# Optimization experiments

Hardware: AMD Instinct MI355X
Metric: run time of the kernel (lower is better)

Reference implementation:

```python
import jax, jax.numpy as jnp
import numpy as np

B, N, C = 4, 2048, 768
H = 12
HD = C // H  # 64
SCALE = HD ** -0.5


def setup_inputs() -> dict:
    key = jax.random.key(0)
    ks = jax.random.split(key, 3)
    x = jax.random.normal(ks[0], (B, N, C), dtype=jnp.float32)
    w_qkv = jax.random.normal(ks[1], (C, 3 * C), dtype=jnp.float32) * (C ** -0.5)
    b_qkv = jnp.zeros((3 * C,), dtype=jnp.float32)
    w_proj = jax.random.normal(ks[2], (C, C), dtype=jnp.float32) * (C ** -0.5)
    b_proj = jnp.zeros((C,), dtype=jnp.float32)
    return {"x": x, "w_qkv": w_qkv, "b_qkv": b_qkv, "w_proj": w_proj, "b_proj": b_proj}


def reference(x, w_qkv, b_qkv, w_proj, b_proj):
    # fused QKV projection: [B, N, 3C] -> [3, B, H, N, HD]
    qkv = (x @ w_qkv + b_qkv).reshape(B, N, 3, H, HD).transpose(2, 0, 3, 1, 4)
    q, k, v = qkv[0] * SCALE, qkv[1], qkv[2]
    # scores [B, H, N, N] (Global mixer: no mask)
    attn = jnp.einsum('bhnd,bhmd->bhnm', q, k)
    attn = jax.nn.softmax(attn, axis=-1)
    # attn @ V -> [B, N, C]
    out = jnp.einsum('bhnm,bhmd->bhnd', attn, v).transpose(0, 2, 1, 3).reshape(B, N, C)
    return out @ w_proj + b_proj
```

## Files before the change

kernel.cpp:

```cpp
#include <hip/hip_runtime.h>
#include <hip/hip_bf16.h>
#include <math.h>

#define B_ 4
#define N_ 2048
#define C_ 768
#define H_ 12
#define HD_ 64

typedef short short8 __attribute__((ext_vector_type(8)));
typedef float float16v __attribute__((ext_vector_type(16)));
typedef unsigned short u16;
typedef unsigned int u32;

static __device__ __forceinline__ u16 f2bf(float x) {
    __hip_bfloat16 b = __float2bfloat16(x);
    return *reinterpret_cast<u16*>(&b);
}
#if defined(__has_builtin)
#if __has_builtin(__builtin_amdgcn_exp2f)
#define EXP2F_FAST __builtin_amdgcn_exp2f
#endif
#endif
#ifndef EXP2F_FAST
#define EXP2F_FAST exp2f
#endif
static __device__ __forceinline__ u32 cpk(float lo, float hi) {
    u32 r;
    asm("v_cvt_pk_bf16_f32 %0, %1, %2" : "=v"(r) : "v"(lo), "v"(hi));
    return r;
}
static __device__ __forceinline__ void gload_lds16(const u16* g, u16* l) {
    __builtin_amdgcn_global_load_lds(
        (const __attribute__((address_space(1))) void*)g,
        (__attribute__((address_space(3))) void*)l, 16, 0, 0);
}

__global__ __launch_bounds__(256) void cast_bf16_kernel(
    const float* __restrict__ X, u16* __restrict__ Xb, int n4)
{
    int i = blockIdx.x * 256 + threadIdx.x;
    if (i < n4) {
        float4 v = ((const float4*)X)[i];
        uint2 o = make_uint2(cpk(v.x, v.y), cpk(v.z, v.w));
        ((uint2*)Xb)[i] = o;
    }
}

__global__ __launch_bounds__(256) void transpose_cvt_kernel(
    const float* __restrict__ W, u16* __restrict__ Wt, int R, int Cc)
{
    __shared__ float tile[64][65];
    const int t = threadIdx.x;
    const int r0 = blockIdx.y * 64, c0 = blockIdx.x * 64;
    const int tr = t >> 4, tc = (t & 15) * 4;
#pragma unroll
    for (int i = 0; i < 4; i++) {
        float4 v = *(const float4*)(W + (size_t)(r0 + tr + i * 16) * Cc + c0 + tc);
        tile[tr + i * 16][tc + 0] = v.x;
        tile[tr + i * 16][tc + 1] = v.y;
        tile[tr + i * 16][tc + 2] = v.z;
        tile[tr + i * 16][tc + 3] = v.w;
    }
    __syncthreads();
#pragma unroll
    for (int i = 0; i < 4; i++) {
        int n = tr + i * 16;
        int k = tc;
        uint2 o = make_uint2(cpk(tile[k + 0][n], tile[k + 1][n]),
                             cpk(tile[k + 2][n], tile[k + 3][n]));
        *(uint2*)(Wt + (size_t)(c0 + n) * R + r0 + k) = o;
    }
}

template<bool OUT_BF16, bool BIAS_ROW>
__global__ __launch_bounds__(256) void gemm_mfma_kernel(
    const u16* __restrict__ A, int lda,
    const u16* __restrict__ Bt,
    const float* __restrict__ bias,
    void* __restrict__ C, int ldc,
    int K, float scale, int scale_cols)
{
    __shared__ u16 As[128 * 64];
    __shared__ u16 Bs[128 * 64];
    const int t = threadIdx.x;
    const int w = t >> 6, lane = t & 63, ln = lane & 31, e = lane >> 5;
    const int wm = w >> 1, wn = w & 1;
    const int row0 = blockIdx.y * 128, col0 = blockIdx.x * 128;
    const int r_sub = lane >> 3;
    const int cg = (lane & 7) ^ r_sub;

    float16v acc[2][2];
#pragma unroll
    for (int i = 0; i < 16; i++) {
        acc[0][0][i] = 0.f; acc[0][1][i] = 0.f;
        acc[1][0][i] = 0.f; acc[1][1][i] = 0.f;
    }

    for (int k0 = 0; k0 < K; k0 += 64) {
        __syncthreads();
#pragma unroll
        for (int i = 0; i < 4; i++) {
            int rr = w * 32 + i * 8;
            const u16* ga = A + (size_t)(row0 + rr + r_sub) * lda + k0 + cg * 8;
            gload_lds16(ga, As + rr * 64);
            const u16* gb = Bt + (size_t)(col0 + rr + r_sub) * K + k0 + cg * 8;
            gload_lds16(gb, Bs + rr * 64);
        }
        __syncthreads();

#pragma unroll
        for (int ks = 0; ks < 4; ks++) {
            short8 af[2], bf[2];
#pragma unroll
            for (int sm = 0; sm < 2; sm++) {
                int r = wm * 64 + sm * 32 + ln;
                af[sm] = *(const short8*)&As[r * 64 + ((2 * ks + e) ^ (r & 7)) * 8];
            }
#pragma unroll
            for (int sn = 0; sn < 2; sn++) {
                int r = wn * 64 + sn * 32 + ln;
                bf[sn] = *(const short8*)&Bs[r * 64 + ((2 * ks + e) ^ (r & 7)) * 8];
            }
#pragma unroll
            for (int sm = 0; sm < 2; sm++)
#pragma unroll
                for (int sn = 0; sn < 2; sn++)
                    acc[sm][sn] = __builtin_amdgcn_mfma_f32_32x32x16_bf16(
                        af[sm], bf[sn], acc[sm][sn], 0, 0, 0);
        }
    }

    const float sc = (col0 < scale_cols) ? scale : 1.0f;
#pragma unroll
    for (int sm = 0; sm < 2; sm++)
#pragma unroll
        for (int sn = 0; sn < 2; sn++) {
            int col = col0 + wn * 64 + sn * 32 + ln;
            float bvc = BIAS_ROW ? 0.f : bias[col];
#pragma unroll
            for (int reg = 0; reg < 16; reg++) {
                int row = row0 + wm * 64 + sm * 32 + (reg & 3) + 8 * (reg >> 2) + 4 * e;
                float bv = BIAS_ROW ? bias[row] : bvc;
                float v = (acc[sm][sn][reg] + bv) * sc;
                if (OUT_BF16)
                    ((u16*)C)[(size_t)row * ldc + col] = f2bf(v);
                else
                    ((float*)C)[(size_t)row * ldc + col] = v;
            }
        }
}

__global__ __launch_bounds__(256) void attn_kernel(
    const u16* __restrict__ qk, const u16* __restrict__ Vt, u16* __restrict__ Ob)
{
    __shared__ __align__(16) u16 lds_us[17664];

    const int t = threadIdx.x;
    const int w = t >> 6, lane = t & 63, ln = lane & 31, e = lane >> 5;
    const int rt = w & 1, kt = w >> 1;
    const int r_sub = lane >> 3;
    const int cgk = (lane & 7) ^ r_sub;

    const int bid = blockIdx.x;
    const int xcd = bid & 7, j = bid >> 3;
    const int bh = xcd * 6 + (j >> 4);
    const int b = bh / H_, h = bh % H_;
    const int row0 = (j & 15) * 128;

    const u16* kq0 = qk + (size_t)b * N_ * 1536 + 768 + h * 64 + cgk * 8
                        + (size_t)(w * 16 + r_sub) * 1536;
    const u16* kq1 = kq0 + (size_t)8 * 1536;
    const u16* vq0 = Vt + (size_t)(h * 64 + w * 16 + r_sub) * (B_ * N_)
                        + b * N_ + cgk * 8;
    const u16* vq1 = vq0 + (size_t)8 * (B_ * N_);

    {
        u16* Kp = lds_us;
        u16* Vp = lds_us + 4096;
        gload_lds16(kq0, Kp + (w * 16 + 0) * 64);
        gload_lds16(kq1, Kp + (w * 16 + 8) * 64);
        gload_lds16(vq0, Vp + (w * 16 + 0) * 64);
        gload_lds16(vq1, Vp + (w * 16 + 8) * 64);
        kq0 += (size_t)64 * 1536; kq1 += (size_t)64 * 1536;
        vq0 += 64; vq1 += 64;
    }

    short8 qfA[4], qfB[4];
    {
        const u16* qa = qk + (size_t)(b * N_ + row0 + rt * 64 + ln) * 1536 + h * 64;
#pragma unroll
        for (int ks = 0; ks < 4; ks++) {
            qfA[ks] = __builtin_bit_cast(short8, *(const uint4*)(qa + ks * 16 + e * 8));
            qfB[ks] = __builtin_bit_cast(short8, *(const uint4*)(qa + 32 * 1536 + ks * 16 + e * 8));
        }
    }

    float16v accA0, accA1, accB0, accB1;
#pragma unroll
    for (int i = 0; i < 16; i++) { accA0[i] = 0.f; accA1[i] = 0.f; accB0[i] = 0.f; accB1[i] = 0.f; }
    float lA = 0.f, lB = 0.f;

    for (int c = 0; c < N_ / 64; c++) {
        __syncthreads();
        if (c + 1 < N_ / 64) {
            u16* Kp = lds_us + ((c + 1) & 1) * 8192;
            u16* Vp = Kp + 4096;
            gload_lds16(kq0, Kp + (w * 16 + 0) * 64);
            gload_lds16(kq1, Kp + (w * 16 + 8) * 64);
            gload_lds16(vq0, Vp + (w * 16 + 0) * 64);
            gload_lds16(vq1, Vp + (w * 16 + 8) * 64);
            kq0 += (size_t)64 * 1536; kq1 += (size_t)64 * 1536;
            vq0 += 64; vq1 += 64;
        }
        const u16* Ks = lds_us + (c & 1) * 8192;
        const u16* Vs = Ks + 4096;

        float16v sA, sB;
#pragma unroll
        for (int i = 0; i < 16; i++) { sA[i] = 0.f; sB[i] = 0.f; }
        const int krow = kt * 32 + ln;
#pragma unroll
        for (int ks = 0; ks < 4; ks++) {
            int slot = (2 * ks + e) ^ (ln & 7);
            short8 kf = *(const short8*)&Ks[krow * 64 + slot * 8];
            sA = __builtin_amdgcn_mfma_f32_32x32x16_bf16(kf, qfA[ks], sA, 0, 0, 0);
            sB = __builtin_amdgcn_mfma_f32_32x32x16_bf16(kf, qfB[ks], sB, 0, 0, 0);
        }

#pragma unroll
        for (int i = 0; i < 16; i++) {
            sA[i] = EXP2F_FAST(sA[i]);
            sB[i] = EXP2F_FAST(sB[i]);
        }
        {
            float a0 = (sA[0] + sA[1]) + (sA[2] + sA[3]);
            float a1 = (sA[4] + sA[5]) + (sA[6] + sA[7]);
            float a2 = (sA[8] + sA[9]) + (sA[10] + sA[11]);
            float a3 = (sA[12] + sA[13]) + (sA[14] + sA[15]);
            float b0 = (sB[0] + sB[1]) + (sB[2] + sB[3]);
            float b1 = (sB[4] + sB[5]) + (sB[6] + sB[7]);
            float b2 = (sB[8] + sB[9]) + (sB[10] + sB[11]);
            float b3 = (sB[12] + sB[13]) + (sB[14] + sB[15]);
            float la = (a0 + a1) + (a2 + a3);
            float lb = (b0 + b1) + (b2 + b3);
            lA += la + __shfl_xor(la, 32);
            lB += lb + __shfl_xor(lb, 32);
        }

#pragma unroll
        for (int g2 = 0; g2 < 2; g2++) {
            uint4 pA4 = make_uint4(cpk(sA[8 * g2 + 0], sA[8 * g2 + 1]),
                                   cpk(sA[8 * g2 + 2], sA[8 * g2 + 3]),
                                   cpk(sA[8 * g2 + 4], sA[8 * g2 + 5]),
                                   cpk(sA[8 * g2 + 6], sA[8 * g2 + 7]));
            uint4 pB4 = make_uint4(cpk(sB[8 * g2 + 0], sB[8 * g2 + 1]),
                                   cpk(sB[8 * g2 + 2], sB[8 * g2 + 3]),
                                   cpk(sB[8 * g2 + 4], sB[8 * g2 + 5]),
                                   cpk(sB[8 * g2 + 6], sB[8 * g2 + 7]));
            short8 pfA = __builtin_bit_cast(short8, pA4);
            short8 pfB = __builtin_bit_cast(short8, pB4);

            const int c0 = 4 * kt + 2 * g2;
#pragma unroll
            for (int dh = 0; dh < 2; dh++) {
                int d = dh * 32 + ln;
                uint2 r1 = *(const uint2*)&Vs[d * 64 + ((c0 ^ (d & 7)) * 8) + 4 * e];
                uint2 r2 = *(const uint2*)&Vs[d * 64 + (((c0 + 1) ^ (d & 7)) * 8) + 4 * e];
                uint4 va4 = make_uint4(r1.x, r1.y, r2.x, r2.y);
                short8 va = __builtin_bit_cast(short8, va4);
                if (dh == 0) {
                    accA0 = __builtin_amdgcn_mfma_f32_32x32x16_bf16(va, pfA, accA0, 0, 0, 0);
                    accB0 = __builtin_amdgcn_mfma_f32_32x32x16_bf16(va, pfB, accB0, 0, 0, 0);
                } else {
                    accA1 = __builtin_amdgcn_mfma_f32_32x32x16_bf16(va, pfA, accA1, 0, 0, 0);
                    accB1 = __builtin_amdgcn_mfma_f32_32x32x16_bf16(va, pfB, accB1, 0, 0, 0);
                }
            }
        }
    }

    __syncthreads();
    float* Osf = (float*)lds_us;
    float* lred = Osf + 128 * 68;
    const int rowA = rt * 64 + ln, rowB = rt * 64 + 32 + ln;

    if (kt == 1) {
#pragma unroll
        for (int reg = 0; reg < 16; reg++) {
            int d = (reg & 3) + 8 * (reg >> 2) + 4 * e;
            Osf[rowA * 68 + d]      = accA0[reg];
            Osf[rowA * 68 + d + 32] = accA1[reg];
            Osf[rowB * 68 + d]      = accB0[reg];
            Osf[rowB * 68 + d + 32] = accB1[reg];
        }
        lred[rowA] = lA;
        lred[rowB] = lB;
    }
    __syncthreads();
    if (kt == 0) {
        float linvA = 1.0f / (lA + lred[rowA]);
        float linvB = 1.0f / (lB + lred[rowB]);
#pragma unroll
        for (int reg = 0; reg < 16; reg++) {
            int d = (reg & 3) + 8 * (reg >> 2) + 4 * e;
            Osf[rowA * 68 + d]      = (accA0[reg] + Osf[rowA * 68 + d]) * linvA;
            Osf[rowA * 68 + d + 32] = (accA1[reg] + Osf[rowA * 68 + d + 32]) * linvA;
            Osf[rowB * 68 + d]      = (accB0[reg] + Osf[rowB * 68 + d]) * linvB;
            Osf[rowB * 68 + d + 32] = (accB1[reg] + Osf[rowB * 68 + d + 32]) * linvB;
        }
#pragma unroll
        for (int j2 = 0; j2 < 8; j2++) {
            int idx = lane + j2 * 64;
            int r = idx >> 3, gg = idx & 7;
            float4 o0 = *(float4*)&Osf[(rt * 64 + r) * 68 + gg * 8];
            float4 o1 = *(float4*)&Osf[(rt * 64 + r) * 68 + gg * 8 + 4];
            uint4 ov = make_uint4(cpk(o0.x, o0.y), cpk(o0.z, o0.w),
                                  cpk(o1.x, o1.y), cpk(o1.z, o1.w));
            *(uint4*)(Ob + (size_t)(b * N_ + row0 + rt * 64 + r) * 768
                         + h * 64 + gg * 8) = ov;
        }
    }
}

extern "C" void kernel_launch(void* const* d_in, const int* in_sizes, int n_in,
                              void* d_out, int out_size, void* d_ws, size_t ws_size,
                              hipStream_t stream) {
    const float* x      = (const float*)d_in[0];
    const float* w_qkv  = (const float*)d_in[1];
    const float* b_qkv  = (const float*)d_in[2];
    const float* w_proj = (const float*)d_in[3];
    const float* b_proj = (const float*)d_in[4];
    float* out = (float*)d_out;

    char* ws = (char*)d_ws;
    u16* qk2    = (u16*)ws;
    u16* Vt     = (u16*)(ws + 25165824);
    u16* Ob     = (u16*)(ws + 37748736);
    u16* xb     = (u16*)(ws + 50331648);
    u16* wqkvT  = (u16*)(ws + 62914560);
    u16* wprojT = (u16*)(ws + 66453504);

    cast_bf16_kernel<<<6144, 256, 0, stream>>>(x, xb, (B_ * N_ * C_) / 4);
    transpose_cvt_kernel<<<dim3(36, 12), 256, 0, stream>>>(w_qkv, wqkvT, C_, 3 * C_);
    transpose_cvt_kernel<<<dim3(12, 12), 256, 0, stream>>>(w_proj, wprojT, C_, C_);

    gemm_mfma_kernel<true, false><<<dim3(12, 64), 256, 0, stream>>>(
        xb, C_, wqkvT, b_qkv, qk2, 1536, C_, 0.18033688011112042f, 768);

    gemm_mfma_kernel<true, true><<<dim3(64, 6), 256, 0, stream>>>(
        wqkvT + (size_t)1536 * C_, C_, xb, b_qkv + 1536, Vt, B_ * N_, C_, 1.0f, 0);

    attn_kernel<<<768, 256, 0, stream>>>(qk2, Vt, Ob);

    gemm_mfma_kernel<false, false><<<dim3(6, 64), 256, 0, stream>>>(
        Ob, C_, wprojT, b_proj, out, C_, C_, 1.0f, 0);
}
```

Baseline: 234.5 us.

## Load K/V directly from global into registers instead of LDS staging

The attention kernel stops staging K and V tiles in double-buffered shared memory with per-iteration barriers. Each wave now loads its own K rows and V slices straight into registers, prefetching K one iteration ahead, and shared memory is kept only for the final cross-wave reduction. Launch bounds now request three blocks per CU. This removes barriers and LDS traffic but duplicates global loads across waves and uses narrow strided V reads, raising register pressure and memory traffic.

```diff
diff --git a/kernel.cpp b/kernel.cpp
--- a/kernel.cpp
+++ b/kernel.cpp
@@ -151,16 +151,15 @@
         }
 }
 
-__global__ __launch_bounds__(256) void attn_kernel(
+__global__ __launch_bounds__(256, 3) void attn_kernel(
     const u16* __restrict__ qk, const u16* __restrict__ Vt, u16* __restrict__ Ob)
 {
-    __shared__ __align__(16) u16 lds_us[17664];
+    __shared__ float Osf[128 * 68];
+    __shared__ float lred[128];
 
     const int t = threadIdx.x;
     const int w = t >> 6, lane = t & 63, ln = lane & 31, e = lane >> 5;
     const int rt = w & 1, kt = w >> 1;
-    const int r_sub = lane >> 3;
-    const int cgk = (lane & 7) ^ r_sub;
 
     const int bid = blockIdx.x;
     const int xcd = bid & 7, j = bid >> 3;
@@ -168,23 +167,9 @@
     const int b = bh / H_, h = bh % H_;
     const int row0 = (j & 15) * 128;
 
-    const u16* kq0 = qk + (size_t)b * N_ * 1536 + 768 + h * 64 + cgk * 8
-                        + (size_t)(w * 16 + r_sub) * 1536;
-    const u16* kq1 = kq0 + (size_t)8 * 1536;
-    const u16* vq0 = Vt + (size_t)(h * 64 + w * 16 + r_sub) * (B_ * N_)
-                        + b * N_ + cgk * 8;
-    const u16* vq1 = vq0 + (size_t)8 * (B_ * N_);
-
-    {
-        u16* Kp = lds_us;
-        u16* Vp = lds_us + 4096;
-        gload_lds16(kq0, Kp + (w * 16 + 0) * 64);
-        gload_lds16(kq1, Kp + (w * 16 + 8) * 64);
-        gload_lds16(vq0, Vp + (w * 16 + 0) * 64);
-        gload_lds16(vq1, Vp + (w * 16 + 8) * 64);
-        kq0 += (size_t)64 * 1536; kq1 += (size_t)64 * 1536;
-        vq0 += 64; vq1 += 64;
-    }
+    const u16* kp = qk + (size_t)(b * N_ + 32 * kt + ln) * 1536 + 768 + h * 64 + e * 8;
+    const u16* vpl = Vt + (size_t)(h * 64 + ln) * (B_ * N_) + b * N_ + 32 * kt + 4 * e;
+    const u16* vph = vpl + (size_t)32 * (B_ * N_);
 
     short8 qfA[4], qfB[4];
     {
@@ -201,31 +186,50 @@
     for (int i = 0; i < 16; i++) { accA0[i] = 0.f; accA1[i] = 0.f; accB0[i] = 0.f; accB1[i] = 0.f; }
     float lA = 0.f, lB = 0.f;
 
+    uint4 k0 = *(const uint4*)(kp + 0 * 16);
+    uint4 k1 = *(const uint4*)(kp + 1 * 16);
+    uint4 k2 = *(const uint4*)(kp + 2 * 16);
+    uint4 k3 = *(const uint4*)(kp + 3 * 16);
+    kp += (size_t)64 * 1536;
+
     for (int c = 0; c < N_ / 64; c++) {
-        __syncthreads();
+        uint2 vv[2][2][2];
+#pragma unroll
+        for (int dh = 0; dh < 2; dh++) {
+            const u16* vp = dh ? vph : vpl;
+#pragma unroll
+            for (int g2 = 0; g2 < 2; g2++)
+#pragma unroll
+                for (int p = 0; p < 2; p++)
+                    vv[dh][g2][p] = *(const uint2*)(vp + g2 * 16 + p * 8);
+        }
+        vpl += 64; vph += 64;
+
+        float16v sA, sB;
+#pragma unroll
+        for (int i = 0; i < 16; i++) { sA[i] = 0.f; sB[i] = 0.f; }
+        {
+            short8 kf;
+            kf = __builtin_bit_cast(short8, k0);
+            sA = __builtin_amdgcn_mfma_f32_32x32x16_bf16(kf, qfA[0], sA, 0, 0, 0);
+            sB = __builtin_amdgcn_mfma_f32_32x32x16_bf16(kf, qfB[0], sB, 0, 0, 0);
+            kf = __builtin_bit_cast(short8, k1);
+            sA = __builtin_amdgcn_mfma_f32_32x32x16_bf16(kf, qfA[1], sA, 0, 0, 0);
+            sB = __builtin_amdgcn_mfma_f32_32x32x16_bf16(kf, qfB[1], sB, 0, 0, 0);
+            kf = __builtin_bit_cast(short8, k2);
+            sA = __builtin_amdgcn_mfma_f32_32x32x16_bf16(kf, qfA[2], sA, 0, 0, 0);
+            sB = __builtin_amdgcn_mfma_f32_32x32x16_bf16(kf, qfB[2], sB, 0, 0, 0);
+            kf = __builtin_bit_cast(short8, k3);
+            sA = __builtin_amdgcn_mfma_f32_32x32x16_bf16(kf, qfA[3], sA, 0, 0, 0);
+            sB = __builtin_amdgcn_mfma_f32_32x32x16_bf16(kf, qfB[3], sB, 0, 0, 0);
+        }
+
         if (c + 1 < N_ / 64) {
-            u16* Kp = lds_us + ((c + 1) & 1) * 8192;
-            u16* Vp = Kp + 4096;
-            gload_lds16(kq0, Kp + (w * 16 + 0) * 64);
-            gload_lds16(kq1, Kp + (w * 16 + 8) * 64);
-            gload_lds16(vq0, Vp + (w * 16 + 0) * 64);
-            gload_lds16(vq1, Vp + (w * 16 + 8) * 64);
-            kq0 += (size_t)64 * 1536; kq1 += (size_t)64 * 1536;
-            vq0 += 64; vq1 += 64;
-        }
-        const u16* Ks = lds_us + (c & 1) * 8192;
-        const u16* Vs = Ks + 4096;
-
-        float16v sA, sB;
-#pragma unroll
-        for (int i = 0; i < 16; i++) { sA[i] = 0.f; sB[i] = 0.f; }
-        const int krow = kt * 32 + ln;
-#pragma unroll
-        for (int ks = 0; ks < 4; ks++) {
-            int slot = (2 * ks + e) ^ (ln & 7);
-            short8 kf = *(const short8*)&Ks[krow * 64 + slot * 8];
-            sA = __builtin_amdgcn_mfma_f32_32x32x16_bf16(kf, qfA[ks], sA, 0, 0, 0);
-            sB = __builtin_amdgcn_mfma_f32_32x32x16_bf16(kf, qfB[ks], sB, 0, 0, 0);
+            k0 = *(const uint4*)(kp + 0 * 16);
+            k1 = *(const uint4*)(kp + 1 * 16);
+            k2 = *(const uint4*)(kp + 2 * 16);
+            k3 = *(const uint4*)(kp + 3 * 16);
+            kp += (size_t)64 * 1536;
         }
 
 #pragma unroll
@@ -261,13 +265,10 @@
             short8 pfA = __builtin_bit_cast(short8, pA4);
             short8 pfB = __builtin_bit_cast(short8, pB4);
 
-            const int c0 = 4 * kt + 2 * g2;
 #pragma unroll
             for (int dh = 0; dh < 2; dh++) {
-                int d = dh * 32 + ln;
-                uint2 r1 = *(const uint2*)&Vs[d * 64 + ((c0 ^ (d & 7)) * 8) + 4 * e];
-                uint2 r2 = *(const uint2*)&Vs[d * 64 + (((c0 + 1) ^ (d & 7)) * 8) + 4 * e];
-                uint4 va4 = make_uint4(r1.x, r1.y, r2.x, r2.y);
+                uint4 va4 = make_uint4(vv[dh][g2][0].x, vv[dh][g2][0].y,
+                                       vv[dh][g2][1].x, vv[dh][g2][1].y);
                 short8 va = __builtin_bit_cast(short8, va4);
                 if (dh == 0) {
                     accA0 = __builtin_amdgcn_mfma_f32_32x32x16_bf16(va, pfA, accA0, 0, 0, 0);
@@ -280,9 +281,6 @@
         }
     }
 
-    __syncthreads();
-    float* Osf = (float*)lds_us;
-    float* lred = Osf + 128 * 68;
     const int rowA = rt * 64 + ln, rowB = rt * 64 + 32 + ln;
 
     if (kt == 1) {
```

After: 286.8 us. 22.3% more time.
